# Performance work log

Measured on AMD Instinct MI355X. Metric: run time of the kernel, lower is better.

Reference implementation:

```python
import jax, jax.numpy as jnp
import numpy as np
from jax import lax

B, DIM, H, W = 4, 128, 56, 56
NH, NG = 4, 2
CG = DIM // NG   # group channels (64)
HC = DIM // NH   # head channels (32)
KS = 7
ORF = 2.0        # offset_range_factor
EPS = 1e-5

def setup_inputs() -> dict:
    key = jax.random.key(0)
    ks = jax.random.split(key, 8)
    s = 0.05
    def rn(k, shp):
        return jax.random.normal(k, shp, jnp.float32) * s
    return {
        "x":    jax.random.normal(ks[0], (B, DIM, H, W), jnp.float32),
        "dw_w": rn(ks[1], (CG, 1, KS, KS)),   # depthwise conv weight
        "dw_b": jnp.zeros((CG,), jnp.float32),
        "ln_g": jnp.ones((CG,), jnp.float32),
        "ln_b": jnp.zeros((CG,), jnp.float32),
        "off_w": rn(ks[2], (2, CG)),          # 1x1 conv to 2 offset channels, no bias
        "q_w": rn(ks[3], (DIM, DIM)), "q_b": jnp.zeros((DIM,), jnp.float32),
        "k_w": rn(ks[4], (DIM, DIM)), "k_b": jnp.zeros((DIM,), jnp.float32),
        "v_w": rn(ks[5], (DIM, DIM)), "v_b": jnp.zeros((DIM,), jnp.float32),
        "o_w": rn(ks[6], (DIM, DIM)), "o_b": jnp.zeros((DIM,), jnp.float32),
    }

def _grid_sample_bilinear(img, grid):
    # img [N,C,Hi,Wi]; grid [N,Ho,Wo,2] with (x,y) in [-1,1]; align_corners=True, zero padding
    N, C, Hi, Wi = img.shape
    Ho, Wo = grid.shape[1], grid.shape[2]
    gx = (grid[..., 0] + 1.0) * 0.5 * (Wi - 1)
    gy = (grid[..., 1] + 1.0) * 0.5 * (Hi - 1)
    x0 = jnp.floor(gx); y0 = jnp.floor(gy)
    wx1 = gx - x0; wx0 = 1.0 - wx1
    wy1 = gy - y0; wy0 = 1.0 - wy1
    flat = img.reshape(N, C, Hi * Wi)
    def corner(xi, yi, w):
        valid = (xi >= 0) & (xi <= Wi - 1) & (yi >= 0) & (yi <= Hi - 1)
        xc = jnp.clip(xi, 0, Wi - 1).astype(jnp.int32)
        yc = jnp.clip(yi, 0, Hi - 1).astype(jnp.int32)
        idx = (yc * Wi + xc).reshape(N, 1, Ho * Wo)
        vals = jnp.take_along_axis(flat, idx, axis=2)
        return vals * (w * valid).reshape(N, 1, Ho * Wo)
    out = (corner(x0, y0, wx0 * wy0) + corner(x0 + 1.0, y0, wx1 * wy0)
           + corner(x0, y0 + 1.0, wx0 * wy1) + corner(x0 + 1.0, y0 + 1.0, wx1 * wy1))
    return out.reshape(N, C, Ho, Wo)

def reference(x, dw_w, dw_b, ln_g, ln_b, off_w, q_w, q_b, k_w, k_b, v_w, v_b, o_w, o_b):
    Bx = x.shape[0]
    # q projection (1x1 conv)
    q = jnp.einsum('oc,bchw->bohw', q_w, x) + q_b[None, :, None, None]
    # offset branch: depthwise conv -> LayerNorm(channels) -> GELU -> 1x1 conv (2 ch)
    q_off = q.reshape(Bx * NG, CG, H, W)
    h = lax.conv_general_dilated(q_off, dw_w, (1, 1), [(KS // 2, KS // 2)] * 2,
                                 feature_group_count=CG,
                                 dimension_numbers=('NCHW', 'OIHW', 'NCHW'))
    h = h + dw_b[None, :, None, None]
    hn = jnp.moveaxis(h, 1, -1)                       # [BG,H,W,CG]
    mu = hn.mean(-1, keepdims=True)
    var = ((hn - mu) ** 2).mean(-1, keepdims=True)
    hn = (hn - mu) * lax.rsqrt(var + EPS) * ln_g + ln_b
    hn = jax.nn.gelu(hn, approximate=False)
    off = jnp.einsum('pc,bhwc->bphw', off_w, hn)      # [BG,2,Hk,Wk], p=(y,x)
    Hk, Wk = off.shape[2], off.shape[3]
    n = Hk * Wk
    rng = jnp.array([1.0 / Hk, 1.0 / Wk], jnp.float32).reshape(1, 2, 1, 1)
    off = jnp.tanh(off) * rng * ORF
    off = jnp.moveaxis(off, 1, -1)                    # [BG,Hk,Wk,2]
    # normalized reference points (y,x)
    ry = (jnp.arange(Hk, dtype=jnp.float32) + 0.5) / Hk * 2.0 - 1.0
    rx = (jnp.arange(Wk, dtype=jnp.float32) + 0.5) / Wk * 2.0 - 1.0
    ref = jnp.stack(jnp.meshgrid(ry, rx, indexing='ij'), -1)  # [Hk,Wk,2]
    pos = off + ref[None]
    # deformable gather: grid_sample expects (x,y)
    xs = _grid_sample_bilinear(x.reshape(Bx * NG, CG, H, W), pos[..., ::-1])
    xs = xs.reshape(Bx, DIM, n)                       # group-major == channel layout
    k = jnp.einsum('oc,bcn->bon', k_w, xs) + k_b[None, :, None]
    v = jnp.einsum('oc,bcn->bon', v_w, xs) + v_b[None, :, None]
    qh = q.reshape(Bx * NH, HC, H * W)
    kh = k.reshape(Bx * NH, HC, n)
    vh = v.reshape(Bx * NH, HC, n)
    attn = jnp.einsum('bcm,bcn->bmn', qh, kh) * (HC ** -0.5)
    attn = jax.nn.softmax(attn, axis=2)
    out = jnp.einsum('bmn,bcn->bcm', attn, vh).reshape(Bx, DIM, H, W)
    return jnp.einsum('oc,bchw->bohw', o_w, out) + o_b[None, :, None, None]
```

## Files before the change

kernel.cpp:

```cpp
#include <hip/hip_runtime.h>
#include <hip/hip_bf16.h>

#define HW 3136

typedef short s16x8 __attribute__((ext_vector_type(8)));
typedef float f32x4 __attribute__((ext_vector_type(4)));
typedef unsigned short us4 __attribute__((ext_vector_type(4)));
typedef unsigned short us8 __attribute__((ext_vector_type(8)));

__device__ inline unsigned short f2bf(float f) {
  union { float f; unsigned int u; } v; v.f = f;
  unsigned int r = v.u + 0x7fff + ((v.u >> 16) & 1);
  return (unsigned short)(r >> 16);
}
__device__ inline float bf2f(unsigned short b) {
  union { unsigned int u; float f; } v; v.u = (unsigned int)b << 16;
  return v.f;
}

__global__ __launch_bounds__(256) void wconv_kernel(
    const float* __restrict__ w0, const float* __restrict__ w1,
    const float* __restrict__ w2, const float* __restrict__ w3,
    unsigned short* __restrict__ o0, unsigned short* __restrict__ o1,
    unsigned short* __restrict__ o2, unsigned short* __restrict__ o3h,
    unsigned short* __restrict__ o3l) {
  int i = blockIdx.x * 256 + threadIdx.x;
  int y = blockIdx.y;
  if (y < 3) {
    const float* s = (y == 0) ? w0 : (y == 1) ? w1 : w2;
    unsigned short* d = (y == 0) ? o0 : (y == 1) ? o1 : o2;
    d[i] = f2bf(s[i]);
  } else {
    float x = w3[i];
    unsigned short hi = f2bf(x);
    o3h[i] = hi;
    o3l[i] = f2bf(x - bf2f(hi));
  }
}

__global__ __launch_bounds__(128) void gemm_q_kernel(
    const float* __restrict__ x, const unsigned short* __restrict__ Wq,
    const float* __restrict__ bias, float* __restrict__ Outf,
    unsigned short* __restrict__ Outb) {
  int by = blockIdx.y;
  int b = by >> 1, oh = by & 1;
  int t = threadIdx.x;
  int w = t >> 6, l = t & 63;
  int lq = l & 15, h = l >> 4;
  int p = blockIdx.x * 32 + w * 16 + lq;

  union S8 { s16x8 v; unsigned short u[8]; };
  S8 bfr[4];
  const float* xs = x + (size_t)b * 128 * HW + p;
  #pragma unroll
  for (int k = 0; k < 4; ++k)
    #pragma unroll
    for (int j = 0; j < 8; ++j)
      bfr[k].u[j] = f2bf(xs[(size_t)(k * 32 + h * 8 + j) * HW]);

  f32x4 acc[4] = {};
  #pragma unroll
  for (int k = 0; k < 4; ++k) {
    #pragma unroll
    for (int ot = 0; ot < 4; ++ot) {
      int og = oh * 4 + ot;
      s16x8 af = *(const s16x8*)&Wq[(size_t)(og * 16 + lq) * 128 + k * 32 + h * 8];
      acc[ot] = __builtin_amdgcn_mfma_f32_16x16x32_bf16(af, bfr[k].v, acc[ot], 0, 0, 0);
    }
  }

  size_t cb = (size_t)b * 128 * HW;
  #pragma unroll
  for (int ot = 0; ot < 4; ++ot) {
    int og = oh * 4 + ot;
    float4 bv = *(const float4*)&bias[og * 16 + h * 4];
    float r[4] = {acc[ot][0] + bv.x, acc[ot][1] + bv.y,
                  acc[ot][2] + bv.z, acc[ot][3] + bv.w};
    #pragma unroll
    for (int i = 0; i < 4; ++i)
      Outf[cb + (size_t)(og * 16 + h * 4 + i) * HW + p] = r[i];
    const float S = 0.25503968151135f;
    us4 rb;
    #pragma unroll
    for (int i = 0; i < 4; ++i) rb[i] = f2bf(r[i] * S);
    *(us4*)&Outb[((size_t)b * HW + p) * 128 + og * 16 + h * 4] = rb;
  }
}

__global__ __launch_bounds__(128) void gemm_kv_kernel(
    const unsigned short* __restrict__ InT, const unsigned short* __restrict__ Wk,
    const unsigned short* __restrict__ Wv, const float* __restrict__ k_b,
    const float* __restrict__ v_b, unsigned short* __restrict__ kbT,
    unsigned short* __restrict__ vb) {
  int by = blockIdx.y;
  int b = by >> 1, oh = by & 1;
  int t = threadIdx.x;
  int w = t >> 6, l = t & 63;
  int lq = l & 15, h = l >> 4;
  int p = blockIdx.x * 32 + w * 16 + lq;

  s16x8 bfr[4];
  const unsigned short* bsrc = InT + ((size_t)b * HW + p) * 128 + h * 8;
  #pragma unroll
  for (int k = 0; k < 4; ++k) bfr[k] = *(const s16x8*)&bsrc[k * 32];

  {
    f32x4 acc[4] = {};
    #pragma unroll
    for (int k = 0; k < 4; ++k) {
      #pragma unroll
      for (int ot = 0; ot < 4; ++ot) {
        int og = oh * 4 + ot;
        s16x8 af = *(const s16x8*)&Wk[(size_t)(og * 16 + lq) * 128 + k * 32 + h * 8];
        acc[ot] = __builtin_amdgcn_mfma_f32_16x16x32_bf16(af, bfr[k], acc[ot], 0, 0, 0);
      }
    }
    #pragma unroll
    for (int ot = 0; ot < 4; ++ot) {
      int og = oh * 4 + ot;
      float4 bv = *(const float4*)&k_b[og * 16 + h * 4];
      us4 rb;
      #pragma unroll
      for (int i = 0; i < 4; ++i) rb[i] = f2bf(acc[ot][i] + bv[i]);
      *(us4*)&kbT[((size_t)b * HW + p) * 128 + og * 16 + h * 4] = rb;
    }
  }
  {
    f32x4 acc[4] = {};
    #pragma unroll
    for (int k = 0; k < 4; ++k) {
      #pragma unroll
      for (int ot = 0; ot < 4; ++ot) {
        int og = oh * 4 + ot;
        s16x8 af = *(const s16x8*)&Wv[(size_t)(og * 16 + lq) * 128 + k * 32 + h * 8];
        acc[ot] = __builtin_amdgcn_mfma_f32_16x16x32_bf16(af, bfr[k], acc[ot], 0, 0, 0);
      }
    }
    size_t cb = (size_t)b * 128 * HW;
    #pragma unroll
    for (int ot = 0; ot < 4; ++ot) {
      int og = oh * 4 + ot;
      float4 bv = *(const float4*)&v_b[og * 16 + h * 4];
      #pragma unroll
      for (int i = 0; i < 4; ++i)
        vb[cb + (size_t)(og * 16 + h * 4 + i) * HW + p] = f2bf(acc[ot][i] + bv[i]);
    }
  }
}

__global__ __launch_bounds__(128) void o_gemm_kernel(
    const unsigned short* __restrict__ AHi, const unsigned short* __restrict__ ALo,
    const unsigned short* __restrict__ WHi, const unsigned short* __restrict__ WLo,
    const float* __restrict__ bias, float* __restrict__ Outf) {
  int by = blockIdx.y;
  int b = by >> 1, oh = by & 1;
  int t = threadIdx.x;
  int w = t >> 6, l = t & 63;
  int lq = l & 15, h = l >> 4;
  int p = blockIdx.x * 32 + w * 16 + lq;

  s16x8 bH[4], bL[4];
  const unsigned short* bsH = AHi + ((size_t)b * HW + p) * 128 + h * 8;
  const unsigned short* bsL = ALo + ((size_t)b * HW + p) * 128 + h * 8;
  #pragma unroll
  for (int k = 0; k < 4; ++k) {
    bH[k] = *(const s16x8*)&bsH[k * 32];
    bL[k] = *(const s16x8*)&bsL[k * 32];
  }

  f32x4 acc[4] = {};
  #pragma unroll
  for (int k = 0; k < 4; ++k) {
    #pragma unroll
    for (int ot = 0; ot < 4; ++ot) {
      int og = oh * 4 + ot;
      size_t wi = (size_t)(og * 16 + lq) * 128 + k * 32 + h * 8;
      s16x8 aH = *(const s16x8*)&WHi[wi];
      s16x8 aL = *(const s16x8*)&WLo[wi];
      acc[ot] = __builtin_amdgcn_mfma_f32_16x16x32_bf16(aH, bH[k], acc[ot], 0, 0, 0);
      acc[ot] = __builtin_amdgcn_mfma_f32_16x16x32_bf16(aH, bL[k], acc[ot], 0, 0, 0);
      acc[ot] = __builtin_amdgcn_mfma_f32_16x16x32_bf16(aL, bH[k], acc[ot], 0, 0, 0);
    }
  }

  size_t cb = (size_t)b * 128 * HW;
  #pragma unroll
  for (int ot = 0; ot < 4; ++ot) {
    int og = oh * 4 + ot;
    float4 bv = *(const float4*)&bias[og * 16 + h * 4];
    #pragma unroll
    for (int i = 0; i < 4; ++i)
      Outf[cb + (size_t)(og * 16 + h * 4 + i) * HW + p] = acc[ot][i] + bv[i];
  }
}

__global__ __launch_bounds__(1024) void offset_kernel(
    const float* __restrict__ q, const float* __restrict__ dw_w,
    const float* __restrict__ dw_b, const float* __restrict__ ln_g,
    const float* __restrict__ ln_b, const float* __restrict__ off_w,
    float* __restrict__ pos) {
  __shared__ float vs[64][65];
  __shared__ float mu_s[64], rs_s[64];
  __shared__ float part[16][64][2];
  int bg = blockIdx.x, h = blockIdx.y;
  int t = threadIdx.x;
  int b = bg >> 1, g = bg & 1;
  const float* qb = q + ((size_t)b * 128 + (size_t)g * 64) * HW;

  {
    int c = t >> 4;
    int wg = t & 15;
    if (wg < 14) {
      int w0 = wg * 4;
      float a0 = dw_b[c], a1 = a0, a2 = a0, a3 = a0;
      const float* qc = qb + (size_t)c * HW;
      const float* wc = dw_w + c * 49;
      #pragma unroll
      for (int ky = 0; ky < 7; ++ky) {
        int y = h + ky - 3;
        if (y >= 0 && y < 56) {
          float row[10];
          #pragma unroll
          for (int i = 0; i < 10; ++i) {
            int xx = w0 - 3 + i;
            row[i] = (xx >= 0 && xx < 56) ? qc[y * 56 + xx] : 0.f;
          }
          #pragma unroll
          for (int kx = 0; kx < 7; ++kx) {
            float wv = wc[ky * 7 + kx];
            a0 += row[kx] * wv;
            a1 += row[kx + 1] * wv;
            a2 += row[kx + 2] * wv;
            a3 += row[kx + 3] * wv;
          }
        }
      }
      vs[c][w0 + 0] = a0;
      vs[c][w0 + 1] = a1;
      vs[c][w0 + 2] = a2;
      vs[c][w0 + 3] = a3;
    } else {
      int base = 56 + (wg - 14) * 4;
      vs[c][base + 0] = 0.f;
      vs[c][base + 1] = 0.f;
      vs[c][base + 2] = 0.f;
      vs[c][base + 3] = 0.f;
    }
  }
  __syncthreads();

  int w = t & 63;
  int cq = t >> 6;
  if (cq == 0) {
    float sum = 0.f;
    #pragma unroll 8
    for (int c = 0; c < 64; ++c) sum += vs[c][w];
    float mu = sum * 0.015625f;
    float var = 0.f;
    #pragma unroll 8
    for (int c = 0; c < 64; ++c) { float d = vs[c][w] - mu; var += d * d; }
    mu_s[w] = mu;
    rs_s[w] = rsqrtf(var * 0.015625f + 1e-5f);
  }
  __syncthreads();

  {
    float mu = mu_s[w], rstd = rs_s[w];
    float oy = 0.f, ox = 0.f;
    #pragma unroll
    for (int i = 0; i < 4; ++i) {
      int c = cq * 4 + i;
      float hn = (vs[c][w] - mu) * rstd * ln_g[c] + ln_b[c];
      hn = 0.5f * hn * (1.f + erff(hn * 0.70710678118654752f));
      oy += off_w[c] * hn;
      ox += off_w[64 + c] * hn;
    }
    part[cq][w][0] = oy;
    part[cq][w][1] = ox;
  }
  __syncthreads();

  if (cq == 0 && w < 56) {
    float oy = 0.f, ox = 0.f;
    #pragma unroll
    for (int pw = 0; pw < 16; ++pw) {
      oy += part[pw][w][0];
      ox += part[pw][w][1];
    }
    float py = tanhf(oy) * (2.0f / 56.f) + ((h + 0.5f) * (2.f / 56.f) - 1.f);
    float px = tanhf(ox) * (2.0f / 56.f) + ((w + 0.5f) * (2.f / 56.f) - 1.f);
    int idx = bg * HW + h * 56 + w;
    pos[idx * 2 + 0] = (px + 1.f) * 0.5f * 55.f;
    pos[idx * 2 + 1] = (py + 1.f) * 0.5f * 55.f;
  }
}

__global__ __launch_bounds__(256) void sample_kernel(
    const float* __restrict__ x, const float* __restrict__ pos,
    unsigned short* __restrict__ xsT) {
  int t = threadIdx.x;
  int p = blockIdx.x * 64 + (t & 63);
  int cg = t >> 6;
  int bg = p / HW, pp = p % HW;
  int b = bg >> 1, g = bg & 1;
  float gx = pos[2 * p], gy = pos[2 * p + 1];
  float x0f = floorf(gx), y0f = floorf(gy);
  float wx1 = gx - x0f, wx0 = 1.f - wx1;
  float wy1 = gy - y0f, wy0 = 1.f - wy1;
  int x0 = (int)x0f, y0 = (int)y0f;
  int x1 = x0 + 1, y1 = y0 + 1;
  float vx0 = (x0 >= 0 && x0 < 56) ? 1.f : 0.f;
  float vx1 = (x1 >= 0 && x1 < 56) ? 1.f : 0.f;
  float vy0 = (y0 >= 0 && y0 < 56) ? 1.f : 0.f;
  float vy1 = (y1 >= 0 && y1 < 56) ? 1.f : 0.f;
  int xc0 = min(max(x0, 0), 55), xc1 = min(max(x1, 0), 55);
  int yc0 = min(max(y0, 0), 55), yc1 = min(max(y1, 0), 55);
  float w00 = wx0 * wy0 * vx0 * vy0, w10 = wx1 * wy0 * vx1 * vy0;
  float w01 = wx0 * wy1 * vx0 * vy1, w11 = wx1 * wy1 * vx1 * vy1;
  int i00 = yc0 * 56 + xc0, i10 = yc0 * 56 + xc1;
  int i01 = yc1 * 56 + xc0, i11 = yc1 * 56 + xc1;
  const float* xb = x + ((size_t)b * 128 + (size_t)g * 64 + cg * 16) * HW;
  unsigned short tmp[16];
  #pragma unroll 4
  for (int i = 0; i < 16; ++i) {
    const float* xc = xb + (size_t)i * HW;
    tmp[i] = f2bf(w00 * xc[i00] + w10 * xc[i10] + w01 * xc[i01] + w11 * xc[i11]);
  }
  unsigned short* dst = xsT + ((size_t)b * HW + pp) * 128 + g * 64 + cg * 16;
  *(us8*)&dst[0] = *(us8*)&tmp[0];
  *(us8*)&dst[8] = *(us8*)&tmp[8];
}

__global__ __launch_bounds__(128) void attn_mfma_kernel(
    const unsigned short* __restrict__ qT, const unsigned short* __restrict__ kT,
    const unsigned short* __restrict__ vbf, unsigned short* __restrict__ aoHi,
    unsigned short* __restrict__ aoLo) {
  __shared__ __align__(16) unsigned short Klds[2][64][40];
  __shared__ __align__(16) unsigned short Plds[2][2][16][68];
  const int KSTEP = 64 * 40;
  int bh = blockIdx.y;
  int b = bh >> 2, hd = bh & 3;
  int t = threadIdx.x;
  int w = t >> 6, l = t & 63;
  int lq = l & 15, h = l >> 4;
  int q0 = blockIdx.x * 64 + w * 32;
  size_t vbase = (size_t)bh * 32 * HW;

  union S8 { s16x8 v; long long q[2]; unsigned short u[8]; };

  S8 qf0, qf1;
  qf0.v = *(const s16x8*)&qT[((size_t)b * HW + q0 + lq) * 128 + hd * 32 + h * 8];
  qf1.v = *(const s16x8*)&qT[((size_t)b * HW + q0 + 16 + lq) * 128 + hd * 32 + h * 8];

  int srow = t >> 1, sseg = (t & 1) * 16;
  const unsigned short* ksrc =
      kT + ((size_t)b * HW + srow) * 128 + hd * 32 + sseg;
  unsigned short* kdst = &Klds[0][srow][sseg];

  const unsigned short* vl = vbf + vbase + (size_t)lq * HW + h * 8;

  f32x4 oacc0[2] = {{0.f, 0.f, 0.f, 0.f}, {0.f, 0.f, 0.f, 0.f}};
  f32x4 oacc1[2] = {{0.f, 0.f, 0.f, 0.f}, {0.f, 0.f, 0.f, 0.f}};
  float lsum0 = 0.f, lsum1 = 0.f;

  S8 kr0, kr1, vreg[4];
  kr0.v = *(const s16x8*)&ksrc[0];
  kr1.v = *(const s16x8*)&ksrc[8];
  *(s16x8*)&kdst[0] = kr0.v;
  *(s16x8*)&kdst[8] = kr1.v;
  kr0.v = *(const s16x8*)&ksrc[(size_t)64 * 128];
  kr1.v = *(const s16x8*)&ksrc[(size_t)64 * 128 + 8];
  #pragma unroll
  for (int c = 0; c < 2; ++c)
    #pragma unroll
    for (int n = 0; n < 2; ++n)
      vreg[c * 2 + n].v = *(const s16x8*)&vl[(size_t)(n * 16) * HW + c * 32];
  asm volatile("s_waitcnt lgkmcnt(0)" ::: "memory");
  __builtin_amdgcn_s_barrier();

  for (int tix = 0; tix < 49; ++tix) {
    int cur = tix & 1;
    int kbV = (tix + 1 < 49) ? (tix + 1) * 64 : 0;
    int kbK = (tix + 2 < 49) ? (tix + 2) * 64 : 3072;

    f32x4 st0[4], st1[4];
    #pragma unroll
    for (int tt = 0; tt < 4; ++tt) {
      S8 af;
      af.v = *(const s16x8*)&Klds[cur][tt * 16 + lq][h * 8];
      st0[tt] = __builtin_amdgcn_mfma_f32_16x16x32_bf16(
          af.v, qf0.v, (f32x4){0.f, 0.f, 0.f, 0.f}, 0, 0, 0);
      st1[tt] = __builtin_amdgcn_mfma_f32_16x16x32_bf16(
          af.v, qf1.v, (f32x4){0.f, 0.f, 0.f, 0.f}, 0, 0, 0);
    }

    #pragma unroll
    for (int tt = 0; tt < 4; ++tt) {
      float a0, a1, a2, a3, b0, b1, b2, b3;
      asm("v_exp_f32 %0, %1" : "=v"(a0) : "v"(st0[tt][0]));
      asm("v_exp_f32 %0, %1" : "=v"(a1) : "v"(st0[tt][1]));
      asm("v_exp_f32 %0, %1" : "=v"(a2) : "v"(st0[tt][2]));
      asm("v_exp_f32 %0, %1" : "=v"(a3) : "v"(st0[tt][3]));
      asm("v_exp_f32 %0, %1" : "=v"(b0) : "v"(st1[tt][0]));
      asm("v_exp_f32 %0, %1" : "=v"(b1) : "v"(st1[tt][1]));
      asm("v_exp_f32 %0, %1" : "=v"(b2) : "v"(st1[tt][2]));
      asm("v_exp_f32 %0, %1" : "=v"(b3) : "v"(st1[tt][3]));
      lsum0 += (a0 + a1) + (a2 + a3);
      lsum1 += (b0 + b1) + (b2 + b3);
      unsigned int lo0, hi0, lo1, hi1;
      asm("v_cvt_pk_bf16_f32 %0, %1, %2" : "=v"(lo0) : "v"(a0), "v"(a1));
      asm("v_cvt_pk_bf16_f32 %0, %1, %2" : "=v"(hi0) : "v"(a2), "v"(a3));
      asm("v_cvt_pk_bf16_f32 %0, %1, %2" : "=v"(lo1) : "v"(b0), "v"(b1));
      asm("v_cvt_pk_bf16_f32 %0, %1, %2" : "=v"(hi1) : "v"(b2), "v"(b3));
      unsigned long long pk0 = (unsigned long long)lo0 | ((unsigned long long)hi0 << 32);
      unsigned long long pk1 = (unsigned long long)lo1 | ((unsigned long long)hi1 << 32);
      *(unsigned long long*)&Plds[w][0][lq][tt * 16 + h * 4] = pk0;
      *(unsigned long long*)&Plds[w][1][lq][tt * 16 + h * 4] = pk1;
    }

    #pragma unroll
    for (int c = 0; c < 2; ++c) {
      S8 pf0, pf1;
      pf0.q[0] = *(const long long*)&Plds[w][0][lq][c * 32 + h * 8];
      pf0.q[1] = *(const long long*)&Plds[w][0][lq][c * 32 + h * 8 + 4];
      pf1.q[0] = *(const long long*)&Plds[w][1][lq][c * 32 + h * 8];
      pf1.q[1] = *(const long long*)&Plds[w][1][lq][c * 32 + h * 8 + 4];
      #pragma unroll
      for (int n = 0; n < 2; ++n) {
        oacc0[n] = __builtin_amdgcn_mfma_f32_16x16x32_bf16(
            vreg[c * 2 + n].v, pf0.v, oacc0[n], 0, 0, 0);
        oacc1[n] = __builtin_amdgcn_mfma_f32_16x16x32_bf16(
            vreg[c * 2 + n].v, pf1.v, oacc1[n], 0, 0, 0);
      }
    }

    #pragma unroll
    for (int c = 0; c < 2; ++c)
      #pragma unroll
      for (int n = 0; n < 2; ++n)
        vreg[c * 2 + n].v =
            *(const s16x8*)&vl[(size_t)(n * 16) * HW + kbV + c * 32];

    *(s16x8*)(kdst + (cur ^ 1) * KSTEP) = kr0.v;
    *(s16x8*)(kdst + (cur ^ 1) * KSTEP + 8) = kr1.v;
    kr0.v = *(const s16x8*)&ksrc[(size_t)kbK * 128];
    kr1.v = *(const s16x8*)&ksrc[(size_t)kbK * 128 + 8];

    asm volatile("s_waitcnt lgkmcnt(0)" ::: "memory");
    __builtin_amdgcn_s_barrier();
  }

  lsum0 += __shfl_xor(lsum0, 16);
  lsum0 += __shfl_xor(lsum0, 32);
  lsum1 += __shfl_xor(lsum1, 16);
  lsum1 += __shfl_xor(lsum1, 32);
  float inv0 = 1.f / lsum0;
  float inv1 = 1.f / lsum1;
  #pragma unroll
  for (int f = 0; f < 2; ++f) {
    float inv = f ? inv1 : inv0;
    f32x4* oacc = f ? oacc1 : oacc0;
    size_t obase = ((size_t)b * HW + q0 + f * 16 + lq) * 128 + hd * 32;
    #pragma unroll
    for (int n = 0; n < 2; ++n) {
      us4 rh, rl;
      #pragma unroll
      for (int r = 0; r < 4; ++r) {
        float v = oacc[n][r] * inv;
        unsigned short hi = f2bf(v);
        rh[r] = hi;
        rl[r] = f2bf(v - bf2f(hi));
      }
      *(us4*)&aoHi[obase + n * 16 + h * 4] = rh;
      *(us4*)&aoLo[obase + n * 16 + h * 4] = rl;
    }
  }
}

extern "C" void kernel_launch(void* const* d_in, const int* in_sizes, int n_in,
                              void* d_out, int out_size, void* d_ws, size_t ws_size,
                              hipStream_t stream) {
  const float* x    = (const float*)d_in[0];
  const float* dw_w = (const float*)d_in[1];
  const float* dw_b = (const float*)d_in[2];
  const float* ln_g = (const float*)d_in[3];
  const float* ln_b = (const float*)d_in[4];
  const float* offw = (const float*)d_in[5];
  const float* q_w  = (const float*)d_in[6];
  const float* q_b  = (const float*)d_in[7];
  const float* k_w  = (const float*)d_in[8];
  const float* k_b  = (const float*)d_in[9];
  const float* v_w  = (const float*)d_in[10];
  const float* v_b  = (const float*)d_in[11];
  const float* o_w  = (const float*)d_in[12];
  const float* o_b  = (const float*)d_in[13];

  const size_t NE = 1605632;
  float* ws  = (float*)d_ws;
  float* q   = ws;
  float* pos = q + NE;
  unsigned short* xsT  = (unsigned short*)(pos + 50176);
  unsigned short* qbT  = xsT + NE;
  unsigned short* kbT  = qbT + NE;
  unsigned short* vb   = kbT + NE;
  unsigned short* aoHi = vb + NE;
  unsigned short* aoLo = aoHi + NE;
  unsigned short* Wq   = aoLo + NE;
  unsigned short* Wk   = Wq + 16384;
  unsigned short* Wv   = Wk + 16384;
  unsigned short* WoH  = Wv + 16384;
  unsigned short* WoL  = WoH + 16384;
  float* out = (float*)d_out;

  wconv_kernel<<<dim3(64, 4), 256, 0, stream>>>(q_w, k_w, v_w, o_w,
                                                Wq, Wk, Wv, WoH, WoL);
  gemm_q_kernel<<<dim3(98, 8), 128, 0, stream>>>(x, Wq, q_b, q, qbT);
  offset_kernel<<<dim3(8, 56), 1024, 0, stream>>>(q, dw_w, dw_b, ln_g, ln_b, offw, pos);
  sample_kernel<<<dim3(392), 256, 0, stream>>>(x, pos, xsT);
  gemm_kv_kernel<<<dim3(98, 8), 128, 0, stream>>>(xsT, Wk, Wv, k_b, v_b, kbT, vb);
  attn_mfma_kernel<<<dim3(49, 16), 128, 0, stream>>>(qbT, kbT, vb, aoHi, aoLo);
  o_gemm_kernel<<<dim3(98, 8), 128, 0, stream>>>(aoHi, aoLo, WoH, WoL, o_b, out);
}
```

Measured before the change: 136.7 us.

## Fuse bilinear sampling into K/V projection GEMM via shared memory

Merges the deformable sampling kernel with the K/V projection kernel. Each block samples 32 positions across all 128 channels into an LDS tile, then runs the MFMA K and V projections from LDS, with each wave covering 32 output channels over two 16-position fragments. This removes one launch and the round trip of the sampled xsT tensor through global memory. In exchange the grid is smaller (392 blocks instead of 784) and each block serialises the gather and the GEMM.

```diff
diff --git a/kernel.cpp b/kernel.cpp
--- a/kernel.cpp
+++ b/kernel.cpp
@@ -87,63 +87,115 @@
   }
 }
 
-__global__ __launch_bounds__(128) void gemm_kv_kernel(
-    const unsigned short* __restrict__ InT, const unsigned short* __restrict__ Wk,
-    const unsigned short* __restrict__ Wv, const float* __restrict__ k_b,
-    const float* __restrict__ v_b, unsigned short* __restrict__ kbT,
-    unsigned short* __restrict__ vb) {
-  int by = blockIdx.y;
-  int b = by >> 1, oh = by & 1;
+__global__ __launch_bounds__(256) void sample_kv_kernel(
+    const float* __restrict__ x, const float* __restrict__ pos,
+    const unsigned short* __restrict__ Wk, const unsigned short* __restrict__ Wv,
+    const float* __restrict__ k_b, const float* __restrict__ v_b,
+    unsigned short* __restrict__ kbT, unsigned short* __restrict__ vb) {
+  __shared__ __align__(16) unsigned short xls[32][136];
+  int b = blockIdx.y;
+  int p0 = blockIdx.x * 32;
   int t = threadIdx.x;
+
+  {
+    int pl = t & 31;
+    int cg = t >> 5;
+    int g = cg >> 2;
+    int pp = p0 + pl;
+    int pidx = (b * 2 + g) * HW + pp;
+    float gx = pos[2 * pidx], gy = pos[2 * pidx + 1];
+    float x0f = floorf(gx), y0f = floorf(gy);
+    float wx1 = gx - x0f, wx0 = 1.f - wx1;
+    float wy1 = gy - y0f, wy0 = 1.f - wy1;
+    int x0 = (int)x0f, y0 = (int)y0f;
+    int x1 = x0 + 1, y1 = y0 + 1;
+    float vx0 = (x0 >= 0 && x0 < 56) ? 1.f : 0.f;
+    float vx1 = (x1 >= 0 && x1 < 56) ? 1.f : 0.f;
+    float vy0 = (y0 >= 0 && y0 < 56) ? 1.f : 0.f;
+    float vy1 = (y1 >= 0 && y1 < 56) ? 1.f : 0.f;
+    int xc0 = min(max(x0, 0), 55), xc1 = min(max(x1, 0), 55);
+    int yc0 = min(max(y0, 0), 55), yc1 = min(max(y1, 0), 55);
+    float w00 = wx0 * wy0 * vx0 * vy0, w10 = wx1 * wy0 * vx1 * vy0;
+    float w01 = wx0 * wy1 * vx0 * vy1, w11 = wx1 * wy1 * vx1 * vy1;
+    int i00 = yc0 * 56 + xc0, i10 = yc0 * 56 + xc1;
+    int i01 = yc1 * 56 + xc0, i11 = yc1 * 56 + xc1;
+    const float* xb = x + ((size_t)b * 128 + g * 64 + (cg & 3) * 16) * HW;
+    unsigned short tmp[16];
+    #pragma unroll 4
+    for (int i = 0; i < 16; ++i) {
+      const float* xc = xb + (size_t)i * HW;
+      tmp[i] = f2bf(w00 * xc[i00] + w10 * xc[i10] + w01 * xc[i01] + w11 * xc[i11]);
+    }
+    *(us8*)&xls[pl][cg * 16] = *(us8*)&tmp[0];
+    *(us8*)&xls[pl][cg * 16 + 8] = *(us8*)&tmp[8];
+  }
+  __syncthreads();
+
   int w = t >> 6, l = t & 63;
   int lq = l & 15, h = l >> 4;
-  int p = blockIdx.x * 32 + w * 16 + lq;
-
-  s16x8 bfr[4];
-  const unsigned short* bsrc = InT + ((size_t)b * HW + p) * 128 + h * 8;
-  #pragma unroll
-  for (int k = 0; k < 4; ++k) bfr[k] = *(const s16x8*)&bsrc[k * 32];
+
+  s16x8 bfr[2][4];
+  #pragma unroll
+  for (int pf = 0; pf < 2; ++pf)
+    #pragma unroll
+    for (int k = 0; k < 4; ++k)
+      bfr[pf][k] = *(const s16x8*)&xls[pf * 16 + lq][k * 32 + h * 8];
 
   {
-    f32x4 acc[4] = {};
+    f32x4 acc[2][2] = {};
     #pragma unroll
     for (int k = 0; k < 4; ++k) {
       #pragma unroll
-      for (int ot = 0; ot < 4; ++ot) {
-        int og = oh * 4 + ot;
+      for (int ot = 0; ot < 2; ++ot) {
+        int og = w * 2 + ot;
         s16x8 af = *(const s16x8*)&Wk[(size_t)(og * 16 + lq) * 128 + k * 32 + h * 8];
-        acc[ot] = __builtin_amdgcn_mfma_f32_16x16x32_bf16(af, bfr[k], acc[ot], 0, 0, 0);
-      }
-    }
-    #pragma unroll
-    for (int ot = 0; ot < 4; ++ot) {
-      int og = oh * 4 + ot;
+        #pragma unroll
+        for (int pf = 0; pf < 2; ++pf)
+          acc[ot][pf] = __builtin_amdgcn_mfma_f32_16x16x32_bf16(
+              af, bfr[pf][k], acc[ot][pf], 0, 0, 0);
+      }
+    }
+    #pragma unroll
+    for (int ot = 0; ot < 2; ++ot) {
+      int og = w * 2 + ot;
       float4 bv = *(const float4*)&k_b[og * 16 + h * 4];
-      us4 rb;
-      #pragma unroll
-      for (int i = 0; i < 4; ++i) rb[i] = f2bf(acc[ot][i] + bv[i]);
-      *(us4*)&kbT[((size_t)b * HW + p) * 128 + og * 16 + h * 4] = rb;
+      #pragma unroll
+      for (int pf = 0; pf < 2; ++pf) {
+        int p = p0 + pf * 16 + lq;
+        us4 rb;
+        #pragma unroll
+        for (int i = 0; i < 4; ++i) rb[i] = f2bf(acc[ot][pf][i] + bv[i]);
+        *(us4*)&kbT[((size_t)b * HW + p) * 128 + og * 16 + h * 4] = rb;
+      }
     }
   }
   {
-    f32x4 acc[4] = {};
+    f32x4 acc[2][2] = {};
     #pragma unroll
     for (int k = 0; k < 4; ++k) {
       #pragma unroll
-      for (int ot = 0; ot < 4; ++ot) {
-        int og = oh * 4 + ot;
+      for (int ot = 0; ot < 2; ++ot) {
+        int og = w * 2 + ot;
         s16x8 af = *(const s16x8*)&Wv[(size_t)(og * 16 + lq) * 128 + k * 32 + h * 8];
-        acc[ot] = __builtin_amdgcn_mfma_f32_16x16x32_bf16(af, bfr[k], acc[ot], 0, 0, 0);
+        #pragma unroll
+        for (int pf = 0; pf < 2; ++pf)
+          acc[ot][pf] = __builtin_amdgcn_mfma_f32_16x16x32_bf16(
+              af, bfr[pf][k], acc[ot][pf], 0, 0, 0);
       }
     }
     size_t cb = (size_t)b * 128 * HW;
     #pragma unroll
-    for (int ot = 0; ot < 4; ++ot) {
-      int og = oh * 4 + ot;
+    for (int ot = 0; ot < 2; ++ot) {
+      int og = w * 2 + ot;
       float4 bv = *(const float4*)&v_b[og * 16 + h * 4];
       #pragma unroll
-      for (int i = 0; i < 4; ++i)
-        vb[cb + (size_t)(og * 16 + h * 4 + i) * HW + p] = f2bf(acc[ot][i] + bv[i]);
+      for (int pf = 0; pf < 2; ++pf) {
+        int p = p0 + pf * 16 + lq;
+        #pragma unroll
+        for (int i = 0; i < 4; ++i)
+          vb[cb + (size_t)(og * 16 + h * 4 + i) * HW + p] =
+              f2bf(acc[ot][pf][i] + bv[i]);
+      }
     }
   }
 }
@@ -293,42 +345,6 @@
     pos[idx * 2 + 0] = (px + 1.f) * 0.5f * 55.f;
     pos[idx * 2 + 1] = (py + 1.f) * 0.5f * 55.f;
   }
-}
-
-__global__ __launch_bounds__(256) void sample_kernel(
-    const float* __restrict__ x, const float* __restrict__ pos,
-    unsigned short* __restrict__ xsT) {
-  int t = threadIdx.x;
-  int p = blockIdx.x * 64 + (t & 63);
-  int cg = t >> 6;
-  int bg = p / HW, pp = p % HW;
-  int b = bg >> 1, g = bg & 1;
-  float gx = pos[2 * p], gy = pos[2 * p + 1];
-  float x0f = floorf(gx), y0f = floorf(gy);
-  float wx1 = gx - x0f, wx0 = 1.f - wx1;
-  float wy1 = gy - y0f, wy0 = 1.f - wy1;
-  int x0 = (int)x0f, y0 = (int)y0f;
-  int x1 = x0 + 1, y1 = y0 + 1;
-  float vx0 = (x0 >= 0 && x0 < 56) ? 1.f : 0.f;
-  float vx1 = (x1 >= 0 && x1 < 56) ? 1.f : 0.f;
-  float vy0 = (y0 >= 0 && y0 < 56) ? 1.f : 0.f;
-  float vy1 = (y1 >= 0 && y1 < 56) ? 1.f : 0.f;
-  int xc0 = min(max(x0, 0), 55), xc1 = min(max(x1, 0), 55);
-  int yc0 = min(max(y0, 0), 55), yc1 = min(max(y1, 0), 55);
-  float w00 = wx0 * wy0 * vx0 * vy0, w10 = wx1 * wy0 * vx1 * vy0;
-  float w01 = wx0 * wy1 * vx0 * vy1, w11 = wx1 * wy1 * vx1 * vy1;
-  int i00 = yc0 * 56 + xc0, i10 = yc0 * 56 + xc1;
-  int i01 = yc1 * 56 + xc0, i11 = yc1 * 56 + xc1;
-  const float* xb = x + ((size_t)b * 128 + (size_t)g * 64 + cg * 16) * HW;
-  unsigned short tmp[16];
-  #pragma unroll 4
-  for (int i = 0; i < 16; ++i) {
-    const float* xc = xb + (size_t)i * HW;
-    tmp[i] = f2bf(w00 * xc[i00] + w10 * xc[i10] + w01 * xc[i01] + w11 * xc[i11]);
-  }
-  unsigned short* dst = xsT + ((size_t)b * HW + pp) * 128 + g * 64 + cg * 16;
-  *(us8*)&dst[0] = *(us8*)&tmp[0];
-  *(us8*)&dst[8] = *(us8*)&tmp[8];
 }
 
 __global__ __launch_bounds__(128) void attn_mfma_kernel(
@@ -499,8 +515,7 @@
   float* ws  = (float*)d_ws;
   float* q   = ws;
   float* pos = q + NE;
-  unsigned short* xsT  = (unsigned short*)(pos + 50176);
-  unsigned short* qbT  = xsT + NE;
+  unsigned short* qbT  = (unsigned short*)(pos + 50176);
   unsigned short* kbT  = qbT + NE;
   unsigned short* vb   = kbT + NE;
   unsigned short* aoHi = vb + NE;
@@ -516,8 +531,7 @@
                                                 Wq, Wk, Wv, WoH, WoL);
   gemm_q_kernel<<<dim3(98, 8), 128, 0, stream>>>(x, Wq, q_b, q, qbT);
   offset_kernel<<<dim3(8, 56), 1024, 0, stream>>>(q, dw_w, dw_b, ln_g, ln_b, offw, pos);
-  sample_kernel<<<dim3(392), 256, 0, stream>>>(x, pos, xsT);
-  gemm_kv_kernel<<<dim3(98, 8), 128, 0, stream>>>(xsT, Wk, Wv, k_b, v_b, kbT, vb);
+  sample_kv_kernel<<<dim3(98, 4), 256, 0, stream>>>(x, pos, Wk, Wv, k_b, v_b, kbT, vb);
   attn_mfma_kernel<<<dim3(49, 16), 128, 0, stream>>>(qbT, kbT, vb, aoHi, aoLo);
   o_gemm_kernel<<<dim3(98, 8), 128, 0, stream>>>(aoHi, aoLo, WoH, WoL, o_b, out);
 }
```

After: 129.2 us. 1.06x faster.
